# Kernel optimization log

Measured on AMD Instinct MI355X. Metric: run time of the kernel, lower is better.

Reference implementation:

```python
import jax, jax.numpy as jnp
import numpy as np

B, S, D_MODEL = 4, 2048, 128
NUM_HEADS, HEAD_DIM = 4, 32
EPS = 1e-6


def setup_inputs() -> dict:
    key = jax.random.key(0)
    ks = jax.random.split(key, 5)
    scale = 1.0 / np.sqrt(D_MODEL)
    return {
        "x": jax.random.normal(ks[0], (B, S, D_MODEL), dtype=jnp.float32),
        "Wq": jax.random.normal(ks[1], (D_MODEL, NUM_HEADS * HEAD_DIM), dtype=jnp.float32) * scale,
        "bq": jnp.zeros((NUM_HEADS * HEAD_DIM,), dtype=jnp.float32),
        "Wk": jax.random.normal(ks[2], (D_MODEL, NUM_HEADS * HEAD_DIM), dtype=jnp.float32) * scale,
        "bk": jnp.zeros((NUM_HEADS * HEAD_DIM,), dtype=jnp.float32),
        "Wv": jax.random.normal(ks[3], (D_MODEL, NUM_HEADS * HEAD_DIM), dtype=jnp.float32) * scale,
        "bv": jnp.zeros((NUM_HEADS * HEAD_DIM,), dtype=jnp.float32),
        "gamma": jnp.ones((D_MODEL,), dtype=jnp.float32),
        "beta": jnp.zeros((D_MODEL,), dtype=jnp.float32),
        "Wo": jax.random.normal(ks[4], (NUM_HEADS * HEAD_DIM, D_MODEL), dtype=jnp.float32) * scale,
        "bo": jnp.zeros((D_MODEL,), dtype=jnp.float32),
    }


def _split_heads(t):
    # [B, S, H*D] -> [B, H, S, D]
    b, s, _ = t.shape
    return t.reshape(b, s, NUM_HEADS, HEAD_DIM).transpose(0, 2, 1, 3)


def reference(x, Wq, bq, Wk, bk, Wv, bv, gamma, beta, Wo, bo):
    # Pre-LayerNorm (Keras LayerNormalization, eps=1e-6)
    mu = jnp.mean(x, axis=-1, keepdims=True)
    var = jnp.mean(jnp.square(x - mu), axis=-1, keepdims=True)
    xn = (x - mu) * jax.lax.rsqrt(var + EPS) * gamma + beta

    q = _split_heads(xn @ Wq + bq)  # [B,H,S,Dh]
    k = _split_heads(xn @ Wk + bk)
    v = _split_heads(xn @ Wv + bv)

    scores = jnp.einsum("bhqd,bhkd->bhqk", q, k) / jnp.sqrt(jnp.float32(HEAD_DIM))
    attn = jax.nn.softmax(scores, axis=-1)  # [B,H,S,S]
    ctx = jnp.einsum("bhqk,bhkd->bhqd", attn, v)  # [B,H,S,Dh]

    # merge heads -> [B,S,H*Dh]
    ctx = ctx.transpose(0, 2, 1, 3).reshape(x.shape[0], x.shape[1], NUM_HEADS * HEAD_DIM)
    out = ctx @ Wo + bo
    return out + x  # residual
```

## Files before the change

kernel.cpp:

```cpp
#include <hip/hip_runtime.h>

#define D_MODEL 128
#define SEQ 2048
#define NH 4
#define DH 32
#define NBATCH 4
#define BHN 16

typedef __attribute__((ext_vector_type(8))) short bf16x8;
typedef __attribute__((ext_vector_type(4))) float f32x4;
typedef __attribute__((ext_vector_type(4))) unsigned short u16x4;
typedef __attribute__((ext_vector_type(8))) unsigned short u16x8;

#define QSCALE (0.17677669529663687f * 1.4426950408889634f)

static __device__ __forceinline__ unsigned short f2bf_rne(float f) {
    union { float f; unsigned int u; } v; v.f = f;
    unsigned int r = v.u + 0x7FFFu + ((v.u >> 16) & 1u);
    return (unsigned short)(r >> 16);
}


__global__ __launch_bounds__(256) void k0_prep(
    const float* __restrict__ Wq, const float* __restrict__ Wk,
    const float* __restrict__ Wv, const float* __restrict__ Wo,
    unsigned short* __restrict__ wf)
{
    int tid = blockIdx.x * 256 + threadIdx.x;
    int nt = tid >> 8, kk = (tid >> 6) & 3, lane = tid & 63;
    int col = lane & 15, quad = lane >> 4;
    const float* W = (nt < 8) ? Wq : (nt < 16) ? Wk : (nt < 24) ? Wv : Wo;
    int n = (nt & 7) * 16 + col;
    u16x8 v;
    #pragma unroll
    for (int j = 0; j < 8; ++j)
        v[j] = f2bf_rne(W[(kk * 32 + quad * 8 + j) * 128 + n]);
    *(u16x8*)(wf + (size_t)tid * 8) = v;
}

__global__ __launch_bounds__(512) void k1_ln_qkv(
    const float* __restrict__ x, const unsigned short* __restrict__ wf,
    const float* __restrict__ bq, const float* __restrict__ bk,
    const float* __restrict__ bv,
    const float* __restrict__ gamma, const float* __restrict__ beta,
    unsigned short* __restrict__ qf_ws, unsigned short* __restrict__ kf_ws,
    unsigned short* __restrict__ vf_ws)
{
    __shared__ __align__(16) unsigned short xsh[32][136];
    __shared__ __align__(16) unsigned short stqk[32][272];
    __shared__ __align__(16) unsigned short stv[128][40];
    const int t = threadIdx.x, w = t >> 6, lane = t & 63;
    const int row0 = blockIdx.x * 32;
    const float g0 = gamma[lane], g1 = gamma[lane + 64];
    const float be0 = beta[lane], be1 = beta[lane + 64];
    #pragma unroll
    for (int i = 0; i < 4; ++i) {
        int r = w * 4 + i;
        const float* xr = x + (size_t)(row0 + r) * 128;
        float x0 = xr[lane], x1 = xr[lane + 64];
        float s = x0 + x1, s2 = x0 * x0 + x1 * x1;
        #pragma unroll
        for (int off = 32; off > 0; off >>= 1) {
            s += __shfl_xor(s, off);
            s2 += __shfl_xor(s2, off);
        }
        float mu  = s * (1.0f / 128.0f);
        float var = s2 * (1.0f / 128.0f) - mu * mu;
        float rs  = rsqrtf(var + 1e-6f);
        xsh[r][lane]      = f2bf_rne((x0 - mu) * rs * g0 + be0);
        xsh[r][lane + 64] = f2bf_rne((x1 - mu) * rs * g1 + be1);
    }
    __syncthreads();

    const int col = lane & 15, quad = lane >> 4;
    const int mt = w & 1, mrow = mt * 16;
    const int nt0 = (w >> 1) * 6;
    bf16x8 a[4];
    #pragma unroll
    for (int kk = 0; kk < 4; ++kk)
        a[kk] = *(const bf16x8*)&xsh[mrow + col][kk * 32 + quad * 8];

    for (int nt = nt0; nt < nt0 + 6; ++nt) {
        int n = nt * 16 + col;
        const unsigned short* wrow = wf + (size_t)(nt * 4) * 512 + lane * 8;
        f32x4 c = {0.f, 0.f, 0.f, 0.f};
        #pragma unroll
        for (int kk = 0; kk < 4; ++kk) {
            bf16x8 bfr = *(const bf16x8*)(wrow + kk * 512);
            c = __builtin_amdgcn_mfma_f32_16x16x32_bf16(a[kk], bfr, c, 0, 0, 0);
        }
        int m = nt >> 3;
        int nn = n & 127;
        if (m < 2) {
            float bias = (m == 0) ? bq[nn] : bk[nn];
            float scale = (m == 0) ? QSCALE : 1.0f;
            #pragma unroll
            for (int r = 0; r < 4; ++r)
                stqk[mrow + quad * 4 + r][n] = f2bf_rne((c[r] + bias) * scale);
        } else {
            float bias = bv[nn];
            u16x4 pv;
            #pragma unroll
            for (int r = 0; r < 4; ++r) pv[r] = f2bf_rne(c[r] + bias);
            *(u16x4*)&stv[nn][mrow + quad * 4] = pv;
        }
    }
    __syncthreads();

    const int b   = row0 >> 11;
    const int kbi = (row0 & (SEQ - 1)) >> 5;
    const int h   = w >> 1, par = w & 1;
    const int bh  = b * NH + h;
    {
        u16x8 qv = *(const u16x8*)&stqk[par * 16 + col][h * 32 + quad * 8];
        int qi = ((row0 & (SEQ - 1)) >> 4) + par;
        *(u16x8*)(qf_ws + (size_t)(bh * 128 + qi) * 512 + lane * 8) = qv;
    }
    {
        u16x8 kv = *(const u16x8*)&stqk[2 * col + par][128 + h * 32 + quad * 8];
        *(u16x8*)(kf_ws + ((size_t)(bh * 64 + kbi) * 2 + par) * 512 + lane * 8) = kv;
    }
    {
        u16x8 vv = *(const u16x8*)&stv[h * 32 + par * 16 + col][quad * 8];
        *(u16x8*)(vf_ws + ((size_t)(bh * 64 + kbi) * 2 + par) * 512 + lane * 8) = vv;
    }
}

__global__ __launch_bounds__(1024) void k23_attn_out(
    const unsigned short* __restrict__ qf_ws,
    const unsigned short* __restrict__ kf_ws,
    const unsigned short* __restrict__ vf_ws,
    const unsigned short* __restrict__ wf,
    const float* __restrict__ bo, const float* __restrict__ x,
    float* __restrict__ out)
{
    __shared__ __align__(16) float comb[16][32][33];
    __shared__ float lsh[16][32];
    __shared__ __align__(16) unsigned short ctx_sh[32][136];

    const int w = threadIdx.x >> 6, lane = threadIdx.x & 63;
    const int col = lane & 15, quad = lane >> 4;
    const int h = w >> 2, kh = w & 3;
    const int b = blockIdx.y;
    const int bh = b * NH + h;
    const int q0 = blockIdx.x * 32;
    const int qi = blockIdx.x * 2;

    const unsigned short* qb = qf_ws + (size_t)(bh * 128 + qi) * 512;
    const unsigned short* kb0 = kf_ws + (size_t)bh * 65536 + (size_t)(kh * 16) * 1024;
    const unsigned short* vb0 = vf_ws + (size_t)bh * 65536 + (size_t)(kh * 16) * 1024;

    bf16x8 qf0 = *(const bf16x8*)(qb + lane * 8);
    bf16x8 qf1 = *(const bf16x8*)(qb + 512 + lane * 8);

    f32x4 c00 = {0.f,0.f,0.f,0.f}, c01 = {0.f,0.f,0.f,0.f};
    f32x4 c10 = {0.f,0.f,0.f,0.f}, c11 = {0.f,0.f,0.f,0.f};
    float l0 = 0.f, l1 = 0.f;

    const unsigned short* pk = kb0;
    const unsigned short* pv = vb0;
    bf16x8 kf0 = *(const bf16x8*)(pk + lane * 8);
    bf16x8 kf1 = *(const bf16x8*)(pk + 512 + lane * 8);
    bf16x8 vf0 = *(const bf16x8*)(pv + lane * 8);
    bf16x8 vf1 = *(const bf16x8*)(pv + 512 + lane * 8);

    for (int it = 0; it < 16; ++it) {
        const unsigned short* nk = (it == 15) ? kb0 : pk + 1024;
        const unsigned short* nv = (it == 15) ? vb0 : pv + 1024;
        bf16x8 nkf0 = *(const bf16x8*)(nk + lane * 8);
        bf16x8 nkf1 = *(const bf16x8*)(nk + 512 + lane * 8);
        bf16x8 nvf0 = *(const bf16x8*)(nv + lane * 8);
        bf16x8 nvf1 = *(const bf16x8*)(nv + 512 + lane * 8);

        f32x4 z = {0.f,0.f,0.f,0.f};
        f32x4 s00 = __builtin_amdgcn_mfma_f32_16x16x32_bf16(kf0, qf0, z, 0, 0, 0);
        f32x4 s01 = __builtin_amdgcn_mfma_f32_16x16x32_bf16(kf1, qf0, z, 0, 0, 0);
        f32x4 s10 = __builtin_amdgcn_mfma_f32_16x16x32_bf16(kf0, qf1, z, 0, 0, 0);
        f32x4 s11 = __builtin_amdgcn_mfma_f32_16x16x32_bf16(kf1, qf1, z, 0, 0, 0);

        union { bf16x8 v; unsigned int u[4]; } pf0, pf1;
        #pragma unroll
        for (int r = 0; r < 4; ++r) {
            float pe = __builtin_amdgcn_exp2f(s00[r]);
            float po = __builtin_amdgcn_exp2f(s01[r]);
            l0 += pe + po;
            pf0.u[r] = (__float_as_uint(pe) >> 16) | (__float_as_uint(po) & 0xFFFF0000u);
            float qe = __builtin_amdgcn_exp2f(s10[r]);
            float qo = __builtin_amdgcn_exp2f(s11[r]);
            l1 += qe + qo;
            pf1.u[r] = (__float_as_uint(qe) >> 16) | (__float_as_uint(qo) & 0xFFFF0000u);
        }
        c00 = __builtin_amdgcn_mfma_f32_16x16x32_bf16(pf0.v, vf0, c00, 0, 0, 0);
        c01 = __builtin_amdgcn_mfma_f32_16x16x32_bf16(pf0.v, vf1, c01, 0, 0, 0);
        c10 = __builtin_amdgcn_mfma_f32_16x16x32_bf16(pf1.v, vf0, c10, 0, 0, 0);
        c11 = __builtin_amdgcn_mfma_f32_16x16x32_bf16(pf1.v, vf1, c11, 0, 0, 0);
        kf0 = nkf0; kf1 = nkf1; vf0 = nvf0; vf1 = nvf1;
        pk = nk; pv = nv;
    }

    l0 += __shfl_xor(l0, 16); l0 += __shfl_xor(l0, 32);
    l1 += __shfl_xor(l1, 16); l1 += __shfl_xor(l1, 32);

    #pragma unroll
    for (int r = 0; r < 4; ++r) {
        int rr = quad * 4 + r;
        comb[w][rr][col]           = c00[r];
        comb[w][rr][16 + col]      = c01[r];
        comb[w][16 + rr][col]      = c10[r];
        comb[w][16 + rr][16 + col] = c11[r];
    }
    if (quad == 0) {
        lsh[w][col]      = l0;
        lsh[w][16 + col] = l1;
    }
    __syncthreads();

    {
        int row = threadIdx.x >> 5;
        int dg  = (threadIdx.x & 31) * 4;
        int hh  = dg >> 5;
        int wb  = hh * 4;
        float linv = 1.0f / (lsh[wb][row] + lsh[wb + 1][row]
                           + lsh[wb + 2][row] + lsh[wb + 3][row]);
        int dl = dg & 31;
        u16x4 ov;
        #pragma unroll
        for (int j = 0; j < 4; ++j)
            ov[j] = f2bf_rne((comb[wb][row][dl + j] + comb[wb + 1][row][dl + j]
                            + comb[wb + 2][row][dl + j] + comb[wb + 3][row][dl + j])
                             * linv);
        *(u16x4*)&ctx_sh[row][dg] = ov;
    }
    __syncthreads();

    {
        int nt = w & 7, mt = w >> 3;
        bf16x8 a[4];
        #pragma unroll
        for (int kk = 0; kk < 4; ++kk)
            a[kk] = *(const bf16x8*)&ctx_sh[mt * 16 + col][kk * 32 + quad * 8];
        int n = nt * 16 + col;
        int nt_g = 24 + nt;
        f32x4 c = {0.f, 0.f, 0.f, 0.f};
        #pragma unroll
        for (int kk = 0; kk < 4; ++kk) {
            bf16x8 bfr = *(const bf16x8*)(wf + ((size_t)(nt_g * 4 + kk) * 64 + lane) * 8);
            c = __builtin_amdgcn_mfma_f32_16x16x32_bf16(a[kk], bfr, c, 0, 0, 0);
        }
        float bias = bo[n];
        #pragma unroll
        for (int r = 0; r < 4; ++r) {
            size_t row_g = (size_t)b * SEQ + q0 + mt * 16 + quad * 4 + r;
            out[row_g * 128 + n] = c[r] + bias + x[row_g * 128 + n];
        }
    }
}

extern "C" void kernel_launch(void* const* d_in, const int* in_sizes, int n_in,
                              void* d_out, int out_size, void* d_ws, size_t ws_size,
                              hipStream_t stream) {
    const float* x     = (const float*)d_in[0];
    const float* Wq    = (const float*)d_in[1];
    const float* bq    = (const float*)d_in[2];
    const float* Wk    = (const float*)d_in[3];
    const float* bk    = (const float*)d_in[4];
    const float* Wv    = (const float*)d_in[5];
    const float* bv    = (const float*)d_in[6];
    const float* gamma = (const float*)d_in[7];
    const float* beta  = (const float*)d_in[8];
    const float* Wo    = (const float*)d_in[9];
    const float* bo    = (const float*)d_in[10];
    float* out = (float*)d_out;

    const size_t QKV_ELEMS = (size_t)BHN * SEQ * DH;
    unsigned short* qf_ws = (unsigned short*)d_ws;
    unsigned short* kf_ws = qf_ws + QKV_ELEMS;
    unsigned short* vf_ws = kf_ws + QKV_ELEMS;
    unsigned short* wf    = vf_ws + QKV_ELEMS;

    k0_prep<<<32, 256, 0, stream>>>(Wq, Wk, Wv, Wo, wf);
    k1_ln_qkv<<<256, 512, 0, stream>>>(x, wf, bq, bk, bv, gamma, beta,
                                       qf_ws, kf_ws, vf_ws);
    k23_attn_out<<<dim3(64, 4), 1024, 0, stream>>>(qf_ws, kf_ws, vf_ws, wf,
                                                   bo, x, out);
}
```

Before: 101.1 us.

## Fuse weight bf16 conversion into consumer kernels and add MFMA priority hints

```diff
diff --git a/kernel.cpp b/kernel.cpp
--- a/kernel.cpp
+++ b/kernel.cpp
@@ -21,35 +21,22 @@
 }
 
 
-__global__ __launch_bounds__(256) void k0_prep(
+__global__ __launch_bounds__(512) void k1_ln_qkv(
+    const float* __restrict__ x,
     const float* __restrict__ Wq, const float* __restrict__ Wk,
-    const float* __restrict__ Wv, const float* __restrict__ Wo,
-    unsigned short* __restrict__ wf)
-{
-    int tid = blockIdx.x * 256 + threadIdx.x;
-    int nt = tid >> 8, kk = (tid >> 6) & 3, lane = tid & 63;
-    int col = lane & 15, quad = lane >> 4;
-    const float* W = (nt < 8) ? Wq : (nt < 16) ? Wk : (nt < 24) ? Wv : Wo;
-    int n = (nt & 7) * 16 + col;
-    u16x8 v;
-    #pragma unroll
-    for (int j = 0; j < 8; ++j)
-        v[j] = f2bf_rne(W[(kk * 32 + quad * 8 + j) * 128 + n]);
-    *(u16x8*)(wf + (size_t)tid * 8) = v;
-}
-
-__global__ __launch_bounds__(512) void k1_ln_qkv(
-    const float* __restrict__ x, const unsigned short* __restrict__ wf,
+    const float* __restrict__ Wv,
     const float* __restrict__ bq, const float* __restrict__ bk,
     const float* __restrict__ bv,
     const float* __restrict__ gamma, const float* __restrict__ beta,
     unsigned short* __restrict__ qf_ws, unsigned short* __restrict__ kf_ws,
     unsigned short* __restrict__ vf_ws)
 {
+    __shared__ __align__(16) unsigned short wsh[96 * 512];
     __shared__ __align__(16) unsigned short xsh[32][136];
     __shared__ __align__(16) unsigned short stqk[32][272];
     __shared__ __align__(16) unsigned short stv[128][40];
     const int t = threadIdx.x, w = t >> 6, lane = t & 63;
+    const int col = lane & 15, quad = lane >> 4;
     const int row0 = blockIdx.x * 32;
     const float g0 = gamma[lane], g1 = gamma[lane + 64];
     const float be0 = beta[lane], be1 = beta[lane + 64];
@@ -70,9 +57,21 @@
         xsh[r][lane]      = f2bf_rne((x0 - mu) * rs * g0 + be0);
         xsh[r][lane + 64] = f2bf_rne((x1 - mu) * rs * g1 + be1);
     }
-    __syncthreads();
-
-    const int col = lane & 15, quad = lane >> 4;
+
+    #pragma unroll
+    for (int i = 0; i < 12; ++i) {
+        int u = w * 12 + i;
+        int nt = u >> 2, kk = u & 3;
+        const float* W = (nt < 8) ? Wq : (nt < 16) ? Wk : Wv;
+        int n = (nt & 7) * 16 + col;
+        u16x8 v;
+        #pragma unroll
+        for (int j = 0; j < 8; ++j)
+            v[j] = f2bf_rne(W[(kk * 32 + quad * 8 + j) * 128 + n]);
+        *(u16x8*)&wsh[(size_t)u * 512 + lane * 8] = v;
+    }
+    __syncthreads();
+
     const int mt = w & 1, mrow = mt * 16;
     const int nt0 = (w >> 1) * 6;
     bf16x8 a[4];
@@ -82,11 +81,10 @@
 
     for (int nt = nt0; nt < nt0 + 6; ++nt) {
         int n = nt * 16 + col;
-        const unsigned short* wrow = wf + (size_t)(nt * 4) * 512 + lane * 8;
         f32x4 c = {0.f, 0.f, 0.f, 0.f};
         #pragma unroll
         for (int kk = 0; kk < 4; ++kk) {
-            bf16x8 bfr = *(const bf16x8*)(wrow + kk * 512);
+            bf16x8 bfr = *(const bf16x8*)&wsh[(size_t)(nt * 4 + kk) * 512 + lane * 8];
             c = __builtin_amdgcn_mfma_f32_16x16x32_bf16(a[kk], bfr, c, 0, 0, 0);
         }
         int m = nt >> 3;
@@ -130,10 +128,11 @@
     const unsigned short* __restrict__ qf_ws,
     const unsigned short* __restrict__ kf_ws,
     const unsigned short* __restrict__ vf_ws,
-    const unsigned short* __restrict__ wf,
+    const float* __restrict__ Wo,
     const float* __restrict__ bo, const float* __restrict__ x,
     float* __restrict__ out)
 {
+    __shared__ __align__(16) unsigned short wo_sh[32 * 512];
     __shared__ __align__(16) float comb[16][32][33];
     __shared__ float lsh[16][32];
     __shared__ __align__(16) unsigned short ctx_sh[32][136];
@@ -146,6 +145,18 @@
     const int q0 = blockIdx.x * 32;
     const int qi = blockIdx.x * 2;
 
+    #pragma unroll
+    for (int i = 0; i < 2; ++i) {
+        int u = w * 2 + i;
+        int nt = u >> 2, kk = u & 3;
+        int n = nt * 16 + col;
+        u16x8 vv;
+        #pragma unroll
+        for (int j = 0; j < 8; ++j)
+            vv[j] = f2bf_rne(Wo[(kk * 32 + quad * 8 + j) * 128 + n]);
+        *(u16x8*)&wo_sh[(size_t)u * 512 + lane * 8] = vv;
+    }
+
     const unsigned short* qb = qf_ws + (size_t)(bh * 128 + qi) * 512;
     const unsigned short* kb0 = kf_ws + (size_t)bh * 65536 + (size_t)(kh * 16) * 1024;
     const unsigned short* vb0 = vf_ws + (size_t)bh * 65536 + (size_t)(kh * 16) * 1024;
@@ -173,10 +184,12 @@
         bf16x8 nvf1 = *(const bf16x8*)(nv + 512 + lane * 8);
 
         f32x4 z = {0.f,0.f,0.f,0.f};
+        __builtin_amdgcn_s_setprio(1);
         f32x4 s00 = __builtin_amdgcn_mfma_f32_16x16x32_bf16(kf0, qf0, z, 0, 0, 0);
         f32x4 s01 = __builtin_amdgcn_mfma_f32_16x16x32_bf16(kf1, qf0, z, 0, 0, 0);
         f32x4 s10 = __builtin_amdgcn_mfma_f32_16x16x32_bf16(kf0, qf1, z, 0, 0, 0);
         f32x4 s11 = __builtin_amdgcn_mfma_f32_16x16x32_bf16(kf1, qf1, z, 0, 0, 0);
+        __builtin_amdgcn_s_setprio(0);
 
         union { bf16x8 v; unsigned int u[4]; } pf0, pf1;
         #pragma unroll
@@ -190,10 +203,12 @@
             l1 += qe + qo;
             pf1.u[r] = (__float_as_uint(qe) >> 16) | (__float_as_uint(qo) & 0xFFFF0000u);
         }
+        __builtin_amdgcn_s_setprio(1);
         c00 = __builtin_amdgcn_mfma_f32_16x16x32_bf16(pf0.v, vf0, c00, 0, 0, 0);
         c01 = __builtin_amdgcn_mfma_f32_16x16x32_bf16(pf0.v, vf1, c01, 0, 0, 0);
         c10 = __builtin_amdgcn_mfma_f32_16x16x32_bf16(pf1.v, vf0, c10, 0, 0, 0);
         c11 = __builtin_amdgcn_mfma_f32_16x16x32_bf16(pf1.v, vf1, c11, 0, 0, 0);
+        __builtin_amdgcn_s_setprio(0);
         kf0 = nkf0; kf1 = nkf1; vf0 = nvf0; vf1 = nvf1;
         pk = nk; pv = nv;
     }
@@ -240,11 +255,10 @@
         for (int kk = 0; kk < 4; ++kk)
             a[kk] = *(const bf16x8*)&ctx_sh[mt * 16 + col][kk * 32 + quad * 8];
         int n = nt * 16 + col;
-        int nt_g = 24 + nt;
         f32x4 c = {0.f, 0.f, 0.f, 0.f};
         #pragma unroll
         for (int kk = 0; kk < 4; ++kk) {
-            bf16x8 bfr = *(const bf16x8*)(wf + ((size_t)(nt_g * 4 + kk) * 64 + lane) * 8);
+            bf16x8 bfr = *(const bf16x8*)&wo_sh[(size_t)(nt * 4 + kk) * 512 + lane * 8];
             c = __builtin_amdgcn_mfma_f32_16x16x32_bf16(a[kk], bfr, c, 0, 0, 0);
         }
         float bias = bo[n];
@@ -276,11 +290,9 @@
     unsigned short* qf_ws = (unsigned short*)d_ws;
     unsigned short* kf_ws = qf_ws + QKV_ELEMS;
     unsigned short* vf_ws = kf_ws + QKV_ELEMS;
-    unsigned short* wf    = vf_ws + QKV_ELEMS;
-
-    k0_prep<<<32, 256, 0, stream>>>(Wq, Wk, Wv, Wo, wf);
-    k1_ln_qkv<<<256, 512, 0, stream>>>(x, wf, bq, bk, bv, gamma, beta,
+
+    k1_ln_qkv<<<256, 512, 0, stream>>>(x, Wq, Wk, Wv, bq, bk, bv, gamma, beta,
                                        qf_ws, kf_ws, vf_ws);
-    k23_attn_out<<<dim3(64, 4), 1024, 0, stream>>>(qf_ws, kf_ws, vf_ws, wf,
+    k23_attn_out<<<dim3(64, 4), 1024, 0, stream>>>(qf_ws, kf_ws, vf_ws, Wo,
                                                    bo, x, out);
 }
```

New measurement: 100.2 us (median of 2 runs). About the same (-0.9%).
